# Optimization experiments

Hardware: AMD Instinct MI355X
Metric: run time of the kernel (lower is better)

The kernel has to match this reference:

```python
import jax, jax.numpy as jnp
import numpy as np

B, L, S, D_MODEL, H = 4, 2048, 2048, 512, 8
E = D_MODEL // H  # head dim = 64


def setup_inputs() -> dict:
    key = jax.random.key(0)
    ks = jax.random.split(key, 11)
    s = 1.0 / np.sqrt(D_MODEL)
    return {
        "queries": jax.random.normal(ks[0], (B, L, D_MODEL), jnp.float32),
        "keys": jax.random.normal(ks[1], (B, S, D_MODEL), jnp.float32),
        "values": jax.random.normal(ks[2], (B, S, D_MODEL), jnp.float32),
        "Wq": jax.random.normal(ks[3], (D_MODEL, D_MODEL), jnp.float32) * s,
        "bq": jnp.zeros((D_MODEL,), jnp.float32),
        "Wk": jax.random.normal(ks[4], (D_MODEL, D_MODEL), jnp.float32) * s,
        "bk": jnp.zeros((D_MODEL,), jnp.float32),
        "Wv": jax.random.normal(ks[5], (D_MODEL, D_MODEL), jnp.float32) * s,
        "bv": jnp.zeros((D_MODEL,), jnp.float32),
        "Wo": jax.random.normal(ks[6], (D_MODEL, D_MODEL), jnp.float32) * s,
        "bo": jnp.zeros((D_MODEL,), jnp.float32),
    }


def reference(queries, keys, values, Wq, bq, Wk, bk, Wv, bv, Wo, bo):
    # QKV projections, then split heads: [B, T, H, E]
    q = (queries @ Wq + bq).reshape(B, L, H, E)
    k = (keys @ Wk + bk).reshape(B, S, H, E)
    v = (values @ Wv + bv).reshape(B, S, H, E)
    scale = 1.0 / np.sqrt(E)
    # Naive full attention: materialized [B, H, L, S] scores (as in original)
    scores = jnp.einsum('blhe,bshe->bhls', q, k)
    A = jax.nn.softmax(scale * scores, axis=-1)  # dropout = identity at eval
    out = jnp.einsum('bhls,bshd->blhd', A, v).reshape(B, L, H * E)
    return out @ Wo + bo
```

## Files before the change

### kernel.cpp

```cpp
#include <hip/hip_runtime.h>
#include <hip/hip_bf16.h>


typedef __attribute__((ext_vector_type(8))) short bf8_t;
typedef __attribute__((ext_vector_type(4))) float f4_t;
typedef __attribute__((ext_vector_type(16))) float f16_t;
typedef __attribute__((ext_vector_type(4))) unsigned int u32x4;

#define D_MODEL 512
#define HEADS 8
#define EDIM 64
#define LSEQ 2048
#define NBATCH 4
#define MTOT (NBATCH * LSEQ)
#define N4 (MTOT * D_MODEL / 4)

static __device__ __forceinline__ unsigned short f2bf(float f) {
  union { float f; unsigned int u; } x;
  x.f = f;
  unsigned int u = x.u;
  u += 0x7FFFu + ((u >> 16) & 1u);
  return (unsigned short)(u >> 16);
}

static __device__ __forceinline__ unsigned int pack2bf(float a, float b) {
  union { __hip_bfloat162 h; unsigned int u; } c;
  c.h.x = __float2bfloat16(a);
  c.h.y = __float2bfloat16(b);
  return c.u;
}

#define GLOAD_LDS(gptr, lptr)                                                        \
  __builtin_amdgcn_global_load_lds((const __attribute__((address_space(1))) void*)(gptr), \
                                   (__attribute__((address_space(3))) void*)(lptr), 16, 0, 0)

__global__ void cvt_all(const float* __restrict__ q, const float* __restrict__ k,
                        const float* __restrict__ v,
                        unsigned short* __restrict__ Xq, unsigned short* __restrict__ Xk,
                        unsigned short* __restrict__ Xv) {
  int i = blockIdx.x * blockDim.x + threadIdx.x;
  int which = i >> 20;
  int idx = i & (N4 - 1);
  const float* in = (which == 0) ? q : (which == 1) ? k : v;
  unsigned short* out = (which == 0) ? Xq : (which == 1) ? Xk : Xv;
  float4 x = ((const float4*)in)[idx];
  ushort4 o;
  o.x = f2bf(x.x); o.y = f2bf(x.y); o.z = f2bf(x.z); o.w = f2bf(x.w);
  ((ushort4*)out)[idx] = o;
}

__global__ void wt_cvt_all(const float* __restrict__ Wq, const float* __restrict__ Wk,
                           const float* __restrict__ Wv, const float* __restrict__ Wo,
                           unsigned short* __restrict__ Wqt, unsigned short* __restrict__ Wkt,
                           unsigned short* __restrict__ Wvt, unsigned short* __restrict__ Wot) {
  __shared__ float tile[64][65];
  const int which = blockIdx.z;
  const float* W = (which == 0) ? Wq : (which == 1) ? Wk : (which == 2) ? Wv : Wo;
  unsigned short* Wt = (which == 0) ? Wqt : (which == 1) ? Wkt : (which == 2) ? Wvt : Wot;
  const int k0 = blockIdx.x * 64, n0 = blockIdx.y * 64;
  const int tx = threadIdx.x & 63;
  const int ty = threadIdx.x >> 6;
#pragma unroll
  for (int i = 0; i < 64; i += 4)
    tile[i + ty][tx] = W[(size_t)(k0 + i + ty) * D_MODEL + n0 + tx];
  __syncthreads();
#pragma unroll
  for (int i = 0; i < 64; i += 4)
    Wt[(size_t)(n0 + i + ty) * D_MODEL + k0 + tx] = f2bf(tile[tx][i + ty]);
}

__device__ __forceinline__ void stage_a(const unsigned short* __restrict__ A,
                                        unsigned short* lA, int m0, int k0) {
  const int t = threadIdx.x;
  int rowA = t >> 2, cbA = (t & 3) * 16;
  GLOAD_LDS((const char*)(A + (size_t)(m0 + rowA) * D_MODEL + k0) + cbA, (char*)lA + t * 16);
}
__device__ __forceinline__ void stage_b(const unsigned short* __restrict__ Bt,
                                        unsigned short* lB, int n0, int k0) {
  const int t = threadIdx.x;
#pragma unroll
  for (int ii = 0; ii < 2; ++ii) {
    int c = t + ii * 256;
    int rowB = c >> 2, cbB = (c & 3) * 16;
    GLOAD_LDS((const char*)(Bt + (size_t)(n0 + rowB) * D_MODEL + k0) + cbB, (char*)lB + c * 16);
  }
}

__device__ __forceinline__ void gemm_core(const unsigned short* __restrict__ A,
                                          const unsigned short* __restrict__ Bt,
                                          unsigned short* __restrict__ lAv,
                                          unsigned short* __restrict__ lBv,
                                          f4_t (&acc)[2][4], int m0, int n0) {
  const int t = threadIdx.x;
  const int lane = t & 63;
  const int w = t >> 6;
  const int wr = w >> 1, wc = w & 1;
  const int r = lane & 15, g = lane >> 4;
  const int ASZ = 64 * 32, BSZ = 128 * 32;

  stage_a(A, lAv, m0, 0);
  stage_b(Bt, lBv, n0, 0);
  __syncthreads();

  int cur = 0;
  const int NK = D_MODEL / 32;
  for (int ks = 0; ks < NK; ++ks) {
    if (ks + 1 < NK) {
      const int kn = (ks + 1) * 32;
      stage_a(A, lAv + (cur ^ 1) * ASZ, m0, kn);
      stage_b(Bt, lBv + (cur ^ 1) * BSZ, n0, kn);
    }

    bf8_t af[2], bfv[4];
    const unsigned short* lA = lAv + cur * ASZ;
#pragma unroll
    for (int mi = 0; mi < 2; ++mi)
      af[mi] = *(const bf8_t*)(lA + (wr * 32 + mi * 16 + r) * 32 + g * 8);
    const unsigned short* lB = lBv + cur * BSZ;
#pragma unroll
    for (int ni = 0; ni < 4; ++ni)
      bfv[ni] = *(const bf8_t*)(lB + (wc * 64 + ni * 16 + r) * 32 + g * 8);
#pragma unroll
    for (int mi = 0; mi < 2; ++mi)
#pragma unroll
      for (int ni = 0; ni < 4; ++ni)
        acc[mi][ni] = __builtin_amdgcn_mfma_f32_16x16x32_bf16(af[mi], bfv[ni], acc[mi][ni], 0, 0, 0);
    __syncthreads();
    cur ^= 1;
  }
}

#define QSCALE 0.18033688011112042f
__global__ __launch_bounds__(256, 6) void qkv_gemm(
    const unsigned short* __restrict__ Xq, const unsigned short* __restrict__ Xk,
    const unsigned short* __restrict__ Xv,
    const unsigned short* __restrict__ Wqt, const unsigned short* __restrict__ Wkt,
    const unsigned short* __restrict__ Wvt,
    const float* __restrict__ bq, const float* __restrict__ bk, const float* __restrict__ bv,
    unsigned short* __restrict__ Qh, unsigned short* __restrict__ Kh,
    unsigned short* __restrict__ Vt) {
  __shared__ alignas(16) unsigned short lA[2][64 * 32];
  __shared__ alignas(16) unsigned short lB[2][128 * 32];
  const int p = blockIdx.x;
  const int res = p & 7, q = p >> 3;
  const int xx = q & 3;
  const int grp = res + ((q >> 2) << 3);
  const int z = grp >> 7;
  const int y = grp & 127;
  const int n0 = xx * 128, m0 = y * 64;

  const unsigned short* A  = (z == 0) ? Xq : (z == 1) ? Xk : Xv;
  const unsigned short* Bt = (z == 0) ? Wqt : (z == 1) ? Wkt : Wvt;
  const float* bias        = (z == 0) ? bq : (z == 1) ? bk : bv;

  f4_t acc[2][4] = {};
  gemm_core(A, Bt, &lA[0][0], &lB[0][0], acc, m0, n0);

  const int lane = threadIdx.x & 63;
  const int w = threadIdx.x >> 6;
  const int wr = w >> 1, wc = w & 1;
  const int r = lane & 15, g = lane >> 4;
#pragma unroll
  for (int mi = 0; mi < 2; ++mi)
#pragma unroll
    for (int ni = 0; ni < 4; ++ni) {
      const int coln = n0 + wc * 64 + ni * 16 + r;
      const float bv_ = bias[coln];
      const int h = coln >> 6, e = coln & 63;
#pragma unroll
      for (int j = 0; j < 4; ++j) {
        const int rowm = m0 + wr * 32 + mi * 16 + g * 4 + j;
        const int b = rowm >> 11, li = rowm & 2047;
        float v = acc[mi][ni][j] + bv_;
        if (z == 0) {
          v *= QSCALE;
          Qh[(((size_t)(b * HEADS + h) * LSEQ + li) << 6) + e] = f2bf(v);
        } else if (z == 1) {
          Kh[(((size_t)(b * HEADS + h) * LSEQ + li) << 6) + e] = f2bf(v);
        } else {
          Vt[(((size_t)(b * HEADS + h) * EDIM + e) << 11) + li] = f2bf(v);
        }
      }
    }
}

__global__ __launch_bounds__(256, 6) void o_gemm(const unsigned short* __restrict__ A,
                                                 const unsigned short* __restrict__ Bt,
                                                 const float* __restrict__ bias,
                                                 float* __restrict__ Cout) {
  __shared__ alignas(16) unsigned short lA[2][64 * 32];
  __shared__ alignas(16) unsigned short lB[2][128 * 32];
  const int p = blockIdx.x;
  const int res = p & 7, q = p >> 3;
  const int xx = q & 3;
  const int grp = res + ((q >> 2) << 3);
  const int n0 = xx * 128, m0 = grp * 64;

  f4_t acc[2][4] = {};
  gemm_core(A, Bt, &lA[0][0], &lB[0][0], acc, m0, n0);

  const int lane = threadIdx.x & 63;
  const int w = threadIdx.x >> 6;
  const int wr = w >> 1, wc = w & 1;
  const int r = lane & 15, g = lane >> 4;
#pragma unroll
  for (int mi = 0; mi < 2; ++mi)
#pragma unroll
    for (int ni = 0; ni < 4; ++ni) {
      const int coln = n0 + wc * 64 + ni * 16 + r;
      const float bv_ = bias[coln];
#pragma unroll
      for (int j = 0; j < 4; ++j) {
        const int rowm = m0 + wr * 32 + mi * 16 + g * 4 + j;
        Cout[(size_t)rowm * D_MODEL + coln] = acc[mi][ni][j] + bv_;
      }
    }
}

#define XSTR 68

__device__ __forceinline__ void stage_tile(const unsigned short* __restrict__ Kbase,
                                           const unsigned short* __restrict__ Vbase,
                                           unsigned short* ldsK, unsigned short* ldsV,
                                           int s0, int tg) {
#pragma unroll
  for (int ii = 0; ii < 2; ++ii) {
    int c = tg + ii * 256;
    int row = c >> 3, col = c & 7;
    int colp = col ^ (row & 7);
    GLOAD_LDS((const char*)(Kbase + (size_t)(s0 + row) * EDIM + colp * 8),
              (char*)ldsK + c * 16);
    GLOAD_LDS((const char*)(Vbase + (size_t)row * LSEQ + s0 + colp * 8),
              (char*)ldsV + c * 16);
  }
}

__global__ __launch_bounds__(512, 4) void flash_attn(const unsigned short* __restrict__ Qh,
                                                     const unsigned short* __restrict__ Kh,
                                                     const unsigned short* __restrict__ Vt,
                                                     unsigned short* __restrict__ Ao) {
  __shared__ alignas(16) unsigned short stg[2][2][2][64 * 64];

  const int t = threadIdx.x;
  const int lane = t & 63;
  const int w = t >> 6;
  const int wg = w >> 2;
  const int wq = w & 3;
  const int tg = t & 255;
  const int qn = lane & 31;
  const int hi = lane >> 5;
  const int p = blockIdx.x;
  const int xcd = p & 7, jj = p >> 3;
  const int bh = xcd * 4 + (jj >> 4);
  const int qblk = jj & 15;
  const int q0 = qblk * 128 + wq * 32;
  const int sbase = wg * (LSEQ / 2);

  bf8_t qf[4];
#pragma unroll
  for (int kst = 0; kst < 4; ++kst)
    qf[kst] = *(const bf8_t*)(Qh + ((size_t)bh * LSEQ + q0 + qn) * EDIM + kst * 16 + hi * 8);

  float l_lane = 0.f;
  f16_t oacc[2];
#pragma unroll
  for (int eh = 0; eh < 2; ++eh)
#pragma unroll
    for (int r = 0; r < 16; ++r) oacc[eh][r] = 0.f;

  const unsigned short* Kbase = Kh + (size_t)bh * LSEQ * EDIM;
  const unsigned short* Vbase = Vt + (size_t)bh * EDIM * LSEQ;

  stage_tile(Kbase, Vbase, stg[wg][0][0], stg[wg][0][1], sbase, tg);
  __syncthreads();

  int cur = 0;
  const int NT = LSEQ / 2 / 64;
  for (int kt = 0; kt < NT; ++kt) {
    if (kt + 1 < NT)
      stage_tile(Kbase, Vbase, stg[wg][cur ^ 1][0], stg[wg][cur ^ 1][1],
                 sbase + (kt + 1) * 64, tg);

    const unsigned short* lsK = stg[wg][cur][0];
    const unsigned short* lsV = stg[wg][cur][1];

    bf8_t kf[2][4];
#pragma unroll
    for (int sh = 0; sh < 2; ++sh)
#pragma unroll
      for (int kst = 0; kst < 4; ++kst) {
        const int row = 32 * sh + qn;
        const int ch = (2 * kst + hi) ^ (row & 7);
        kf[sh][kst] = *(const bf8_t*)(&lsK[row * 64 + ch * 8]);
      }
    f16_t sacc[2];
#pragma unroll
    for (int sh = 0; sh < 2; ++sh)
#pragma unroll
      for (int r = 0; r < 16; ++r) sacc[sh][r] = 0.f;
#pragma unroll
    for (int sh = 0; sh < 2; ++sh)
#pragma unroll
      for (int kst = 0; kst < 4; ++kst)
        sacc[sh] = __builtin_amdgcn_mfma_f32_32x32x16_bf16(kf[sh][kst], qf[kst], sacc[sh], 0, 0, 0);

    unsigned int pk[16];
#pragma unroll
    for (int sh = 0; sh < 2; ++sh)
#pragma unroll
      for (int i = 0; i < 8; ++i) {
        const float a = __builtin_amdgcn_exp2f(sacc[sh][2 * i]);
        const float b = __builtin_amdgcn_exp2f(sacc[sh][2 * i + 1]);
        l_lane += a + b;
        pk[sh * 8 + i] = pack2bf(a, b);
      }

    unsigned int sw[16];
#pragma unroll
    for (int i = 0; i < 16; ++i) sw[i] = __shfl_xor(pk[i], 32);

    bf8_t pvb[4];
#pragma unroll
    for (int t2 = 0; t2 < 4; ++t2) {
      union { u32x4 u; bf8_t b; } pb;
      pb.u[0] = hi ? sw[4 * t2 + 2] : pk[4 * t2 + 0];
      pb.u[1] = hi ? sw[4 * t2 + 3] : pk[4 * t2 + 1];
      pb.u[2] = hi ? pk[4 * t2 + 2] : sw[4 * t2 + 0];
      pb.u[3] = hi ? pk[4 * t2 + 3] : sw[4 * t2 + 1];
      pvb[t2] = pb.b;
    }

#pragma unroll
    for (int eh = 0; eh < 2; ++eh)
#pragma unroll
      for (int t2 = 0; t2 < 4; ++t2) {
        const int row = 32 * eh + qn;
        const int ch = (2 * t2 + hi) ^ (row & 7);
        const bf8_t vf = *(const bf8_t*)(&lsV[row * 64 + ch * 8]);
        oacc[eh] = __builtin_amdgcn_mfma_f32_32x32x16_bf16(vf, pvb[t2], oacc[eh], 0, 0, 0);
      }

    __syncthreads();
    cur ^= 1;
  }

  const float l_own = l_lane + __shfl_xor(l_lane, 32);
  float* xO = (float*)&stg[0][0][0][0];
  float* xL = xO + 128 * XSTR;

  if (wg == 1) {
#pragma unroll
    for (int eh = 0; eh < 2; ++eh)
#pragma unroll
      for (int k = 0; k < 4; ++k) {
        float4 v4;
        v4.x = oacc[eh][4 * k + 0]; v4.y = oacc[eh][4 * k + 1];
        v4.z = oacc[eh][4 * k + 2]; v4.w = oacc[eh][4 * k + 3];
        *(float4*)(xO + (wq * 32 + qn) * XSTR + 32 * eh + 8 * k + 4 * hi) = v4;
      }
    if (hi == 0) xL[wq * 32 + qn] = l_own;
  }
  __syncthreads();

  if (wg == 0) {
    const float inv = 1.f / (l_own + xL[wq * 32 + qn]);
    const int b = bh >> 3, h = bh & 7;
#pragma unroll
    for (int eh = 0; eh < 2; ++eh)
#pragma unroll
      for (int k = 0; k < 4; ++k) {
        const float4 v4 = *(const float4*)(xO + (wq * 32 + qn) * XSTR + 32 * eh + 8 * k + 4 * hi);
        ushort4 ov;
        ov.x = f2bf((oacc[eh][4 * k + 0] + v4.x) * inv);
        ov.y = f2bf((oacc[eh][4 * k + 1] + v4.y) * inv);
        ov.z = f2bf((oacc[eh][4 * k + 2] + v4.z) * inv);
        ov.w = f2bf((oacc[eh][4 * k + 3] + v4.w) * inv);
        const int e = 32 * eh + 8 * k + 4 * hi;
        *(ushort4*)(Ao + ((size_t)(b * LSEQ + q0 + qn)) * D_MODEL + h * EDIM + e) = ov;
      }
  }
}

extern "C" void kernel_launch(void* const* d_in, const int* in_sizes, int n_in,
                              void* d_out, int out_size, void* d_ws, size_t ws_size,
                              hipStream_t stream) {
  const float* queries = (const float*)d_in[0];
  const float* keys    = (const float*)d_in[1];
  const float* values  = (const float*)d_in[2];
  const float* Wq = (const float*)d_in[3];
  const float* bq = (const float*)d_in[4];
  const float* Wk = (const float*)d_in[5];
  const float* bk = (const float*)d_in[6];
  const float* Wv = (const float*)d_in[7];
  const float* bv = (const float*)d_in[8];
  const float* Wo = (const float*)d_in[9];
  const float* bo = (const float*)d_in[10];

  char* ws = (char*)d_ws;
  const size_t XSZ = (size_t)MTOT * D_MODEL * 2;
  unsigned short* Xq  = (unsigned short*)(ws + 0 * XSZ);
  unsigned short* Xk  = (unsigned short*)(ws + 1 * XSZ);
  unsigned short* Xv  = (unsigned short*)(ws + 2 * XSZ);
  unsigned short* Qh  = (unsigned short*)(ws + 3 * XSZ);
  unsigned short* Kh  = (unsigned short*)(ws + 4 * XSZ);
  unsigned short* Vt  = (unsigned short*)(ws + 5 * XSZ);
  unsigned short* Ao  = (unsigned short*)(ws + 6 * XSZ);
  unsigned short* Wqt = (unsigned short*)(ws + 7 * XSZ);
  unsigned short* Wkt = Wqt + 512 * 512;
  unsigned short* Wvt = Wkt + 512 * 512;
  unsigned short* Wot = Wvt + 512 * 512;

  cvt_all<<<3 * N4 / 256, 256, 0, stream>>>(queries, keys, values, Xq, Xk, Xv);
  wt_cvt_all<<<dim3(8, 8, 4), 256, 0, stream>>>(Wq, Wk, Wv, Wo, Wqt, Wkt, Wvt, Wot);

  qkv_gemm<<<1536, 256, 0, stream>>>(
      Xq, Xk, Xv, Wqt, Wkt, Wvt, bq, bk, bv, Qh, Kh, Vt);

  flash_attn<<<512, 512, 0, stream>>>(Qh, Kh, Vt, Ao);

  o_gemm<<<512, 256, 0, stream>>>(Ao, Wot, bo, (float*)d_out);
}
```

Baseline: 109.2 us.

## Merge prep kernels and drop P-fragment lane shuffles via split V loads

```diff
diff --git a/kernel.cpp b/kernel.cpp
--- a/kernel.cpp
+++ b/kernel.cpp
@@ -3,6 +3,7 @@
 
 
 typedef __attribute__((ext_vector_type(8))) short bf8_t;
+typedef __attribute__((ext_vector_type(4))) short bf4_t;
 typedef __attribute__((ext_vector_type(4))) float f4_t;
 typedef __attribute__((ext_vector_type(16))) float f16_t;
 typedef __attribute__((ext_vector_type(4))) unsigned int u32x4;
@@ -34,39 +35,43 @@
   __builtin_amdgcn_global_load_lds((const __attribute__((address_space(1))) void*)(gptr), \
                                    (__attribute__((address_space(3))) void*)(lptr), 16, 0, 0)
 
-__global__ void cvt_all(const float* __restrict__ q, const float* __restrict__ k,
-                        const float* __restrict__ v,
-                        unsigned short* __restrict__ Xq, unsigned short* __restrict__ Xk,
-                        unsigned short* __restrict__ Xv) {
-  int i = blockIdx.x * blockDim.x + threadIdx.x;
-  int which = i >> 20;
-  int idx = i & (N4 - 1);
-  const float* in = (which == 0) ? q : (which == 1) ? k : v;
-  unsigned short* out = (which == 0) ? Xq : (which == 1) ? Xk : Xv;
-  float4 x = ((const float4*)in)[idx];
-  ushort4 o;
-  o.x = f2bf(x.x); o.y = f2bf(x.y); o.z = f2bf(x.z); o.w = f2bf(x.w);
-  ((ushort4*)out)[idx] = o;
-}
-
-__global__ void wt_cvt_all(const float* __restrict__ Wq, const float* __restrict__ Wk,
-                           const float* __restrict__ Wv, const float* __restrict__ Wo,
-                           unsigned short* __restrict__ Wqt, unsigned short* __restrict__ Wkt,
-                           unsigned short* __restrict__ Wvt, unsigned short* __restrict__ Wot) {
+__global__ void prep_all(const float* __restrict__ q, const float* __restrict__ k,
+                         const float* __restrict__ v,
+                         const float* __restrict__ Wq, const float* __restrict__ Wk,
+                         const float* __restrict__ Wv, const float* __restrict__ Wo,
+                         unsigned short* __restrict__ Xq, unsigned short* __restrict__ Xk,
+                         unsigned short* __restrict__ Xv,
+                         unsigned short* __restrict__ Wqt, unsigned short* __restrict__ Wkt,
+                         unsigned short* __restrict__ Wvt, unsigned short* __restrict__ Wot) {
   __shared__ float tile[64][65];
-  const int which = blockIdx.z;
-  const float* W = (which == 0) ? Wq : (which == 1) ? Wk : (which == 2) ? Wv : Wo;
-  unsigned short* Wt = (which == 0) ? Wqt : (which == 1) ? Wkt : (which == 2) ? Wvt : Wot;
-  const int k0 = blockIdx.x * 64, n0 = blockIdx.y * 64;
-  const int tx = threadIdx.x & 63;
-  const int ty = threadIdx.x >> 6;
-#pragma unroll
-  for (int i = 0; i < 64; i += 4)
-    tile[i + ty][tx] = W[(size_t)(k0 + i + ty) * D_MODEL + n0 + tx];
-  __syncthreads();
-#pragma unroll
-  for (int i = 0; i < 64; i += 4)
-    Wt[(size_t)(n0 + i + ty) * D_MODEL + k0 + tx] = f2bf(tile[tx][i + ty]);
+  const int blk = blockIdx.x;
+  if (blk < 12288) {
+    int i = blk * 256 + threadIdx.x;
+    int which = i >> 20;
+    int idx = i & (N4 - 1);
+    const float* in = (which == 0) ? q : (which == 1) ? k : v;
+    unsigned short* out = (which == 0) ? Xq : (which == 1) ? Xk : Xv;
+    float4 x = ((const float4*)in)[idx];
+    ushort4 o;
+    o.x = f2bf(x.x); o.y = f2bf(x.y); o.z = f2bf(x.z); o.w = f2bf(x.w);
+    ((ushort4*)out)[idx] = o;
+  } else {
+    const int b = blk - 12288;
+    const int which = b >> 6;
+    const int b2 = b & 63;
+    const int k0 = (b2 >> 3) * 64, n0 = (b2 & 7) * 64;
+    const float* W = (which == 0) ? Wq : (which == 1) ? Wk : (which == 2) ? Wv : Wo;
+    unsigned short* Wt = (which == 0) ? Wqt : (which == 1) ? Wkt : (which == 2) ? Wvt : Wot;
+    const int tx = threadIdx.x & 63;
+    const int ty = threadIdx.x >> 6;
+#pragma unroll
+    for (int i = 0; i < 64; i += 4)
+      tile[i + ty][tx] = W[(size_t)(k0 + i + ty) * D_MODEL + n0 + tx];
+    __syncthreads();
+#pragma unroll
+    for (int i = 0; i < 64; i += 4)
+      Wt[(size_t)(n0 + i + ty) * D_MODEL + k0 + tx] = f2bf(tile[tx][i + ty]);
+  }
 }
 
 __device__ __forceinline__ void stage_a(const unsigned short* __restrict__ A,
@@ -315,18 +320,14 @@
         pk[sh * 8 + i] = pack2bf(a, b);
       }
 
-    unsigned int sw[16];
-#pragma unroll
-    for (int i = 0; i < 16; ++i) sw[i] = __shfl_xor(pk[i], 32);
-
     bf8_t pvb[4];
 #pragma unroll
     for (int t2 = 0; t2 < 4; ++t2) {
       union { u32x4 u; bf8_t b; } pb;
-      pb.u[0] = hi ? sw[4 * t2 + 2] : pk[4 * t2 + 0];
-      pb.u[1] = hi ? sw[4 * t2 + 3] : pk[4 * t2 + 1];
-      pb.u[2] = hi ? pk[4 * t2 + 2] : sw[4 * t2 + 0];
-      pb.u[3] = hi ? pk[4 * t2 + 3] : sw[4 * t2 + 1];
+      pb.u[0] = pk[4 * t2 + 0];
+      pb.u[1] = pk[4 * t2 + 1];
+      pb.u[2] = pk[4 * t2 + 2];
+      pb.u[3] = pk[4 * t2 + 3];
       pvb[t2] = pb.b;
     }
 
@@ -335,9 +336,11 @@
 #pragma unroll
       for (int t2 = 0; t2 < 4; ++t2) {
         const int row = 32 * eh + qn;
-        const int ch = (2 * t2 + hi) ^ (row & 7);
-        const bf8_t vf = *(const bf8_t*)(&lsV[row * 64 + ch * 8]);
-        oacc[eh] = __builtin_amdgcn_mfma_f32_32x32x16_bf16(vf, pvb[t2], oacc[eh], 0, 0, 0);
+        const int rx = row & 7;
+        union { struct { bf4_t lo, hi4; } h; bf8_t v; } vfu;
+        vfu.h.lo  = *(const bf4_t*)(&lsV[row * 64 + (((2 * t2 + 0) ^ rx) << 3) + hi * 4]);
+        vfu.h.hi4 = *(const bf4_t*)(&lsV[row * 64 + (((2 * t2 + 1) ^ rx) << 3) + hi * 4]);
+        oacc[eh] = __builtin_amdgcn_mfma_f32_32x32x16_bf16(vfu.v, pvb[t2], oacc[eh], 0, 0, 0);
       }
 
     __syncthreads();
@@ -410,8 +413,8 @@
   unsigned short* Wvt = Wkt + 512 * 512;
   unsigned short* Wot = Wvt + 512 * 512;
 
-  cvt_all<<<3 * N4 / 256, 256, 0, stream>>>(queries, keys, values, Xq, Xk, Xv);
-  wt_cvt_all<<<dim3(8, 8, 4), 256, 0, stream>>>(Wq, Wk, Wv, Wo, Wqt, Wkt, Wvt, Wot);
+  prep_all<<<12544, 256, 0, stream>>>(queries, keys, values, Wq, Wk, Wv, Wo,
+                                      Xq, Xk, Xv, Wqt, Wkt, Wvt, Wot);
 
   qkv_gemm<<<1536, 256, 0, stream>>>(
       Xq, Xk, Xv, Wqt, Wkt, Wvt, bq, bk, bv, Qh, Kh, Vt);
```

Result: no change. 107.8 us (-1.3%).
